# Performance work log

Hardware: AMD Instinct MI355X
Metric: run time of the kernel (lower is better)

Reference implementation:

```python
import jax, jax.numpy as jnp
import numpy as np

IN_FEATURES = 4096
OUT_FEATURES = 4096
BLOCK_SIZE = 64
P = 0.1          # fraction of blocks kept
N_TOKENS = 8192


def setup_inputs() -> dict:
    key = jax.random.key(0)
    k_x, k_w, k_m, k_b = jax.random.split(key, 4)
    x = jax.random.normal(k_x, (N_TOKENS, IN_FEATURES), dtype=jnp.float32)
    # kaiming_uniform_(a=sqrt(5)) on [out, in] -> bound = 1/sqrt(in_features)
    bound = 1.0 / np.sqrt(IN_FEATURES)
    weight = jax.random.uniform(k_w, (OUT_FEATURES, IN_FEATURES), dtype=jnp.float32,
                                minval=-bound, maxval=bound)
    bias = jax.random.uniform(k_b, (OUT_FEATURES,), dtype=jnp.float32,
                              minval=-bound, maxval=bound)
    # Block-structured 0/1 mask: keep each BLOCK_SIZE x BLOCK_SIZE block with prob P
    nb_out, nb_in = OUT_FEATURES // BLOCK_SIZE, IN_FEATURES // BLOCK_SIZE
    block_keep = (jax.random.uniform(k_m, (nb_out, nb_in)) < P).astype(jnp.float32)
    mask = jnp.repeat(jnp.repeat(block_keep, BLOCK_SIZE, axis=0), BLOCK_SIZE, axis=1)
    return {"input": x, "weight": weight, "bias": bias, "mask": mask}


def reference(input, weight, bias, mask):
    # bsr_dense_mm((W*mask).to_sparse_bsr(), x.T).T + bias == x @ (W*mask).T + bias
    masked_w = weight * mask                      # [out, in]
    return input @ masked_w.T + bias              # [N, out]
```

## Files before the change

### kernel.cpp

```cpp
#include <hip/hip_runtime.h>
#include <hip/hip_fp16.h>
#include <cstdint>

#define IN_F   4096
#define OUT_F  4096
#define BS     64
#define NB     64
#define N_TOK  8192
#define TM     256
#define BK     64
#define NMT    (N_TOK / TM)

typedef __attribute__((ext_vector_type(8))) _Float16       f16x8;
typedef __attribute__((ext_vector_type(8))) unsigned short u16x8;
typedef __attribute__((ext_vector_type(4))) float          f32x4;

#define WS_XT_OFF      32768ull
#define WS_XT_BYTES    (2048ull * 32768ull)
#define WS_WT_OFF      (WS_XT_OFF + WS_XT_BYTES)
#define WS_WT_BYTES    (4096ull * 8192ull)
#define WS_NEEDED      (WS_WT_OFF + WS_WT_BYTES)

__global__ void build_meta_kernel(const float* __restrict__ mask,
                                  int* __restrict__ counts,
                                  int* __restrict__ cols) {
    int br = blockIdx.x;
    int bc = threadIdx.x;
    float v = mask[(size_t)(br * BS) * IN_F + (size_t)bc * BS];
    unsigned long long ball = __ballot(v != 0.0f);
    if (v != 0.0f) {
        int pos = __popcll(ball & ((1ull << bc) - 1ull));
        cols[br * NB + pos] = bc;
    }
    if (bc == 0) counts[br] = __popcll(ball);
}

__device__ __forceinline__ u16x8 cvt_f16x8(const float* v) {
    u16x8 o;
#pragma unroll
    for (int j = 0; j < 8; ++j)
        o[j] = __half_as_ushort(__float2half_rn(v[j]));
    return o;
}

__global__ __launch_bounds__(256)
void convert_x_kernel(const float* __restrict__ x, unsigned short* __restrict__ xt) {
    const int t  = blockIdx.x;
    const int mt = t >> 6, kb = t & 63;
    unsigned short* tile = xt + (size_t)t * 16384;
#pragma unroll
    for (int l = 0; l < 8; ++l) {
        int g    = threadIdx.x + l * 256;
        int row  = g >> 3, slot = g & 7;
        const float* src = x + (size_t)(mt * TM + row) * IN_F + kb * BK + slot * 8;
        float4 v0 = *(const float4*)src;
        float4 v1 = *(const float4*)(src + 4);
        float v[8] = {v0.x, v0.y, v0.z, v0.w, v1.x, v1.y, v1.z, v1.w};
        *(u16x8*)&tile[row * 64 + ((slot ^ (row & 7)) << 3)] = cvt_f16x8(v);
    }
}

__global__ __launch_bounds__(256)
void convert_w_kernel(const float* __restrict__ w,
                      const int* __restrict__ counts,
                      const int* __restrict__ cols,
                      unsigned short* __restrict__ wt) {
    const int br = blockIdx.y, si = blockIdx.x;
    if (si >= counts[br]) return;
    const int kb = cols[br * NB + si];
    unsigned short* tile = wt + (size_t)(br * NB + si) * 4096;
#pragma unroll
    for (int l = 0; l < 2; ++l) {
        int g    = threadIdx.x + l * 256;
        int row  = g >> 3, slot = g & 7;
        const float* src = w + (size_t)(br * BS + row) * IN_F + kb * BK + slot * 8;
        float4 v0 = *(const float4*)src;
        float4 v1 = *(const float4*)(src + 4);
        float v[8] = {v0.x, v0.y, v0.z, v0.w, v1.x, v1.y, v1.z, v1.w};
        *(u16x8*)&tile[row * 64 + ((slot ^ (row & 7)) << 3)] = cvt_f16x8(v);
    }
}

__device__ __forceinline__ void gll16(const void* g, void* l) {
    __builtin_amdgcn_global_load_lds(
        (const __attribute__((address_space(1))) unsigned int*)g,
        (__attribute__((address_space(3))) unsigned int*)l, 16, 0, 0);
}

__global__ __launch_bounds__(256, 2)
void bsr_mfma4_kernel(const unsigned short* __restrict__ xt,
                      const unsigned short* __restrict__ wt,
                      const float* __restrict__ bias,
                      const int*   __restrict__ counts,
                      const int*   __restrict__ cols,
                      float* __restrict__ out) {
    __shared__ unsigned short xs[2][TM * BK];
    __shared__ unsigned short wsb[2][BS * BK];

    const int xcd = blockIdx.x & 7;
    const int j   = blockIdx.x >> 3;
    const int mt  = xcd * 4 + (j >> 6);
    const int br  = j & 63;

    const int tid  = threadIdx.x;
    const int lane = tid & 63;
    const int wv   = tid >> 6;
    const int fr   = lane & 15;
    const int kg   = lane >> 4;

    const int  cnt  = counts[br];
    const int* colp = cols + br * NB;

    f32x4 acc[4][4];
#pragma unroll
    for (int a = 0; a < 4; ++a)
#pragma unroll
        for (int b = 0; b < 4; ++b) acc[a][b] = (f32x4)0.0f;

    const char* xbase = (const char*)xt;
    const char* wbase = (const char*)wt;

    auto stage = [&](int si, int bb) {
        const int kb = colp[si];
        const char* xg = xbase + ((size_t)(mt * 64 + kb) << 15);
        const char* wg = wbase + ((size_t)(br * 64 + si) << 13);
        const int bx = wv * 8192;
#pragma unroll
        for (int q = 0; q < 8; ++q)
            gll16(xg + bx + q * 1024 + lane * 16, (char*)xs[bb] + bx + q * 1024);
        const int bw = wv * 2048;
#pragma unroll
        for (int q = 0; q < 2; ++q)
            gll16(wg + bw + q * 1024 + lane * 16, (char*)wsb[bb] + bw + q * 1024);
    };

    int cur = 0;
    if (cnt > 0) stage(0, 0);
    __syncthreads();

    for (int si = 0; si < cnt; ++si) {
        if (si + 1 < cnt) stage(si + 1, cur ^ 1);

#pragma unroll
        for (int ks = 0; ks < 2; ++ks) {
            f16x8 a[4], b[4];
#pragma unroll
            for (int mr = 0; mr < 4; ++mr) {
                int row = wv * 64 + mr * 16 + fr;
                a[mr] = *(const f16x8*)&xs[cur][row * 64 + (((ks * 4 + kg) ^ (row & 7)) << 3)];
            }
#pragma unroll
            for (int nr = 0; nr < 4; ++nr) {
                int row = nr * 16 + fr;
                b[nr] = *(const f16x8*)&wsb[cur][row * 64 + (((ks * 4 + kg) ^ (row & 7)) << 3)];
            }
#pragma unroll
            for (int mr = 0; mr < 4; ++mr)
#pragma unroll
                for (int nr = 0; nr < 4; ++nr)
                    acc[mr][nr] = __builtin_amdgcn_mfma_f32_16x16x32_f16(
                        a[mr], b[nr], acc[mr][nr], 0, 0, 0);
        }
        __syncthreads();
        cur ^= 1;
    }

    const int mbase = mt * TM;
    const int obase = br * BS;
#pragma unroll
    for (int nr = 0; nr < 4; ++nr) {
        float bv = bias[obase + nr * 16 + fr];
#pragma unroll
        for (int mr = 0; mr < 4; ++mr) {
#pragma unroll
            for (int r = 0; r < 4; ++r) {
                int m = mbase + wv * 64 + mr * 16 + kg * 4 + r;
                out[(size_t)m * OUT_F + obase + nr * 16 + fr] = acc[mr][nr][r] + bv;
            }
        }
    }
}

__global__ __launch_bounds__(256, 3)
void bsr_fused_kernel(const float* __restrict__ x,
                      const float* __restrict__ w,
                      const float* __restrict__ bias,
                      const int*   __restrict__ counts,
                      const int*   __restrict__ cols,
                      float* __restrict__ out) {
    __shared__ unsigned short xs[128 * BK];
    __shared__ unsigned short wsb[BS * BK];

    const int mt   = blockIdx.x;
    const int br   = blockIdx.y;
    const int tid  = threadIdx.x;
    const int lane = tid & 63;
    const int wv   = tid >> 6;
    const int fr   = lane & 15;
    const int kg   = lane >> 4;

    const int mbase = mt * 128;
    const int obase = br * BS;
    const int  cnt  = counts[br];
    const int* colp = cols + br * NB;

    f32x4 acc[2][4];
#pragma unroll
    for (int a = 0; a < 2; ++a)
#pragma unroll
        for (int b = 0; b < 4; ++b) acc[a][b] = (f32x4)0.0f;

    for (int si = 0; si < cnt; ++si) {
        const int kbase = colp[si] * BS;
#pragma unroll
        for (int l = 0; l < 4; ++l) {
            int g = tid + l * 256;
            int row = g >> 3, slot = g & 7;
            const float* src = x + (size_t)(mbase + row) * IN_F + kbase + slot * 8;
            float4 v0 = *(const float4*)src;
            float4 v1 = *(const float4*)(src + 4);
            float v[8] = {v0.x, v0.y, v0.z, v0.w, v1.x, v1.y, v1.z, v1.w};
            *(u16x8*)&xs[row * BK + ((slot ^ (row & 7)) << 3)] = cvt_f16x8(v);
        }
#pragma unroll
        for (int l = 0; l < 2; ++l) {
            int g = tid + l * 256;
            int row = g >> 3, slot = g & 7;
            const float* src = w + (size_t)(obase + row) * IN_F + kbase + slot * 8;
            float4 v0 = *(const float4*)src;
            float4 v1 = *(const float4*)(src + 4);
            float v[8] = {v0.x, v0.y, v0.z, v0.w, v1.x, v1.y, v1.z, v1.w};
            *(u16x8*)&wsb[row * BK + ((slot ^ (row & 7)) << 3)] = cvt_f16x8(v);
        }
        __syncthreads();
#pragma unroll
        for (int ks = 0; ks < 2; ++ks) {
            f16x8 a[2], b[4];
#pragma unroll
            for (int mr = 0; mr < 2; ++mr) {
                int row = wv * 32 + mr * 16 + fr;
                a[mr] = *(const f16x8*)&xs[row * BK + (((ks * 4 + kg) ^ (row & 7)) << 3)];
            }
#pragma unroll
            for (int nr = 0; nr < 4; ++nr) {
                int row = nr * 16 + fr;
                b[nr] = *(const f16x8*)&wsb[row * BK + (((ks * 4 + kg) ^ (row & 7)) << 3)];
            }
#pragma unroll
            for (int mr = 0; mr < 2; ++mr)
#pragma unroll
                for (int nr = 0; nr < 4; ++nr)
                    acc[mr][nr] = __builtin_amdgcn_mfma_f32_16x16x32_f16(
                        a[mr], b[nr], acc[mr][nr], 0, 0, 0);
        }
        __syncthreads();
    }

#pragma unroll
    for (int nr = 0; nr < 4; ++nr) {
        float bv = bias[obase + nr * 16 + fr];
#pragma unroll
        for (int mr = 0; mr < 2; ++mr) {
#pragma unroll
            for (int r = 0; r < 4; ++r) {
                int m = mbase + wv * 32 + mr * 16 + kg * 4 + r;
                out[(size_t)m * OUT_F + obase + nr * 16 + fr] = acc[mr][nr][r] + bv;
            }
        }
    }
}

extern "C" void kernel_launch(void* const* d_in, const int* in_sizes, int n_in,
                              void* d_out, int out_size, void* d_ws, size_t ws_size,
                              hipStream_t stream) {
    const float* x    = (const float*)d_in[0];
    const float* w    = (const float*)d_in[1];
    const float* bias = (const float*)d_in[2];
    const float* mask = (const float*)d_in[3];
    float* out = (float*)d_out;

    int* counts = (int*)d_ws;
    int* cols   = (int*)((char*)d_ws + 256);

    build_meta_kernel<<<NB, 64, 0, stream>>>(mask, counts, cols);

    if (ws_size >= WS_NEEDED) {
        unsigned short* xt = (unsigned short*)((char*)d_ws + WS_XT_OFF);
        unsigned short* wt = (unsigned short*)((char*)d_ws + WS_WT_OFF);
        convert_x_kernel<<<NMT * NB, 256, 0, stream>>>(x, xt);
        convert_w_kernel<<<dim3(NB, NB), 256, 0, stream>>>(w, counts, cols, wt);
        bsr_mfma4_kernel<<<NMT * NB, 256, 0, stream>>>(xt, wt, bias, counts, cols, out);
    } else {
        dim3 grid(N_TOK / 128, NB);
        bsr_fused_kernel<<<grid, 256, 0, stream>>>(x, w, bias, counts, cols, out);
    }
}
```

Baseline: 113.9 us.

## Fuse metadata and conversion kernels, recompute mask ballot in-kernel, reorder GEMM blocks

The separate mask-metadata kernel is removed. Each block now derives the kept column bitmask from the mask with a wave ballot and walks it with ffs. The x and w fp16 conversion kernels are merged into a single launch, and the GEMM block-to-tile mapping is changed so each XCD processes paired m-tiles per output block-row, aiming at better L2 locality. This saves launches and a metadata round-trip, at the cost of every block re-reading 64 mask values.

Measured after the change: 118.1 us. +3.7%, slower.

```diff
diff --git a/kernel.cpp b/kernel.cpp
--- a/kernel.cpp
+++ b/kernel.cpp
@@ -15,26 +15,12 @@
 typedef __attribute__((ext_vector_type(8))) unsigned short u16x8;
 typedef __attribute__((ext_vector_type(4))) float          f32x4;
 
-#define WS_XT_OFF      32768ull
+#define WS_XT_OFF      0ull
 #define WS_XT_BYTES    (2048ull * 32768ull)
 #define WS_WT_OFF      (WS_XT_OFF + WS_XT_BYTES)
 #define WS_WT_BYTES    (4096ull * 8192ull)
 #define WS_NEEDED      (WS_WT_OFF + WS_WT_BYTES)
 
-__global__ void build_meta_kernel(const float* __restrict__ mask,
-                                  int* __restrict__ counts,
-                                  int* __restrict__ cols) {
-    int br = blockIdx.x;
-    int bc = threadIdx.x;
-    float v = mask[(size_t)(br * BS) * IN_F + (size_t)bc * BS];
-    unsigned long long ball = __ballot(v != 0.0f);
-    if (v != 0.0f) {
-        int pos = __popcll(ball & ((1ull << bc) - 1ull));
-        cols[br * NB + pos] = bc;
-    }
-    if (bc == 0) counts[br] = __popcll(ball);
-}
-
 __device__ __forceinline__ u16x8 cvt_f16x8(const float* v) {
     u16x8 o;
 #pragma unroll
@@ -43,41 +29,56 @@
     return o;
 }
 
+__device__ __forceinline__ unsigned long long mask_ballot(
+        const float* __restrict__ mask, int br, int lane) {
+    float mv = mask[(size_t)(br * BS) * IN_F + (size_t)lane * BS];
+    return __ballot(mv != 0.0f);
+}
+
 __global__ __launch_bounds__(256)
-void convert_x_kernel(const float* __restrict__ x, unsigned short* __restrict__ xt) {
-    const int t  = blockIdx.x;
-    const int mt = t >> 6, kb = t & 63;
-    unsigned short* tile = xt + (size_t)t * 16384;
-#pragma unroll
-    for (int l = 0; l < 8; ++l) {
-        int g    = threadIdx.x + l * 256;
-        int row  = g >> 3, slot = g & 7;
-        const float* src = x + (size_t)(mt * TM + row) * IN_F + kb * BK + slot * 8;
-        float4 v0 = *(const float4*)src;
-        float4 v1 = *(const float4*)(src + 4);
-        float v[8] = {v0.x, v0.y, v0.z, v0.w, v1.x, v1.y, v1.z, v1.w};
-        *(u16x8*)&tile[row * 64 + ((slot ^ (row & 7)) << 3)] = cvt_f16x8(v);
-    }
-}
-
-__global__ __launch_bounds__(256)
-void convert_w_kernel(const float* __restrict__ w,
-                      const int* __restrict__ counts,
-                      const int* __restrict__ cols,
-                      unsigned short* __restrict__ wt) {
-    const int br = blockIdx.y, si = blockIdx.x;
-    if (si >= counts[br]) return;
-    const int kb = cols[br * NB + si];
-    unsigned short* tile = wt + (size_t)(br * NB + si) * 4096;
-#pragma unroll
-    for (int l = 0; l < 2; ++l) {
-        int g    = threadIdx.x + l * 256;
-        int row  = g >> 3, slot = g & 7;
-        const float* src = w + (size_t)(br * BS + row) * IN_F + kb * BK + slot * 8;
-        float4 v0 = *(const float4*)src;
-        float4 v1 = *(const float4*)(src + 4);
-        float v[8] = {v0.x, v0.y, v0.z, v0.w, v1.x, v1.y, v1.z, v1.w};
-        *(u16x8*)&tile[row * 64 + ((slot ^ (row & 7)) << 3)] = cvt_f16x8(v);
+void convert_all_kernel(const float* __restrict__ x,
+                        const float* __restrict__ w,
+                        const float* __restrict__ mask,
+                        unsigned short* __restrict__ xt,
+                        unsigned short* __restrict__ wt) {
+    const int b = blockIdx.x;
+    if (b < 2048) {
+        const int xcd = b & 7;
+        const int j   = b >> 3;
+        const int mt  = xcd * 4 + (j >> 6);
+        const int kb  = j & 63;
+        unsigned short* tile = xt + (size_t)(mt * 64 + kb) * 16384;
+#pragma unroll
+        for (int l = 0; l < 8; ++l) {
+            int g    = threadIdx.x + l * 256;
+            int row  = g >> 3, slot = g & 7;
+            const float* src = x + (size_t)(mt * TM + row) * IN_F + kb * BK + slot * 8;
+            float4 v0 = *(const float4*)src;
+            float4 v1 = *(const float4*)(src + 4);
+            float v[8] = {v0.x, v0.y, v0.z, v0.w, v1.x, v1.y, v1.z, v1.w};
+            *(u16x8*)&tile[row * 64 + ((slot ^ (row & 7)) << 3)] = cvt_f16x8(v);
+        }
+    } else {
+        const int wb   = b - 2048;
+        const int br   = wb >> 6, si = wb & 63;
+        const int lane = threadIdx.x & 63;
+        unsigned long long ball = mask_ballot(mask, br, lane);
+        if (si >= __popcll(ball)) return;
+        bool fl = ((ball >> lane) & 1ull) &&
+                  (__popcll(ball & ((1ull << lane) - 1ull)) == si);
+        unsigned long long m2 = __ballot(fl);
+        const int kb = __ffsll(m2) - 1;
+        unsigned short* tile = wt + (size_t)(br * NB + si) * 4096;
+#pragma unroll
+        for (int l = 0; l < 2; ++l) {
+            int g    = threadIdx.x + l * 256;
+            int row  = g >> 3, slot = g & 7;
+            const float* src = w + (size_t)(br * BS + row) * IN_F + kb * BK + slot * 8;
+            float4 v0 = *(const float4*)src;
+            float4 v1 = *(const float4*)(src + 4);
+            float v[8] = {v0.x, v0.y, v0.z, v0.w, v1.x, v1.y, v1.z, v1.w};
+            *(u16x8*)&tile[row * 64 + ((slot ^ (row & 7)) << 3)] = cvt_f16x8(v);
+        }
     }
 }
 
@@ -88,19 +89,21 @@
 }
 
 __global__ __launch_bounds__(256, 2)
-void bsr_mfma4_kernel(const unsigned short* __restrict__ xt,
+void bsr_mfma5_kernel(const unsigned short* __restrict__ xt,
                       const unsigned short* __restrict__ wt,
                       const float* __restrict__ bias,
-                      const int*   __restrict__ counts,
-                      const int*   __restrict__ cols,
+                      const float* __restrict__ mask,
                       float* __restrict__ out) {
     __shared__ unsigned short xs[2][TM * BK];
     __shared__ unsigned short wsb[2][BS * BK];
 
-    const int xcd = blockIdx.x & 7;
-    const int j   = blockIdx.x >> 3;
-    const int mt  = xcd * 4 + (j >> 6);
-    const int br  = j & 63;
+    const int b     = blockIdx.x;
+    const int xcd   = b & 7;
+    const int j     = b >> 3;
+    const int phase = j >> 7;
+    const int idx   = j & 127;
+    const int br    = idx >> 1;
+    const int mt    = xcd * 4 + phase * 2 + (idx & 1);
 
     const int tid  = threadIdx.x;
     const int lane = tid & 63;
@@ -108,20 +111,19 @@
     const int fr   = lane & 15;
     const int kg   = lane >> 4;
 
-    const int  cnt  = counts[br];
-    const int* colp = cols + br * NB;
+    unsigned long long ball = mask_ballot(mask, br, lane);
+    const int cnt = __popcll(ball);
 
     f32x4 acc[4][4];
 #pragma unroll
     for (int a = 0; a < 4; ++a)
 #pragma unroll
-        for (int b = 0; b < 4; ++b) acc[a][b] = (f32x4)0.0f;
+        for (int c = 0; c < 4; ++c) acc[a][c] = (f32x4)0.0f;
 
     const char* xbase = (const char*)xt;
     const char* wbase = (const char*)wt;
 
-    auto stage = [&](int si, int bb) {
-        const int kb = colp[si];
+    auto stage = [&](int kb, int si, int bb) {
         const char* xg = xbase + ((size_t)(mt * 64 + kb) << 15);
         const char* wg = wbase + ((size_t)(br * 64 + si) << 13);
         const int bx = wv * 8192;
@@ -134,16 +136,25 @@
             gll16(wg + bw + q * 1024 + lane * 16, (char*)wsb[bb] + bw + q * 1024);
     };
 
+    unsigned long long rem = ball;
     int cur = 0;
-    if (cnt > 0) stage(0, 0);
+    if (cnt > 0) {
+        int kb0 = __ffsll(rem) - 1;
+        rem &= rem - 1;
+        stage(kb0, 0, 0);
+    }
     __syncthreads();
 
     for (int si = 0; si < cnt; ++si) {
-        if (si + 1 < cnt) stage(si + 1, cur ^ 1);
+        if (si + 1 < cnt) {
+            int kbn = __ffsll(rem) - 1;
+            rem &= rem - 1;
+            stage(kbn, si + 1, cur ^ 1);
+        }
 
 #pragma unroll
         for (int ks = 0; ks < 2; ++ks) {
-            f16x8 a[4], b[4];
+            f16x8 a[4], bfr[4];
 #pragma unroll
             for (int mr = 0; mr < 4; ++mr) {
                 int row = wv * 64 + mr * 16 + fr;
@@ -152,14 +163,14 @@
 #pragma unroll
             for (int nr = 0; nr < 4; ++nr) {
                 int row = nr * 16 + fr;
-                b[nr] = *(const f16x8*)&wsb[cur][row * 64 + (((ks * 4 + kg) ^ (row & 7)) << 3)];
+                bfr[nr] = *(const f16x8*)&wsb[cur][row * 64 + (((ks * 4 + kg) ^ (row & 7)) << 3)];
             }
 #pragma unroll
             for (int mr = 0; mr < 4; ++mr)
 #pragma unroll
                 for (int nr = 0; nr < 4; ++nr)
                     acc[mr][nr] = __builtin_amdgcn_mfma_f32_16x16x32_f16(
-                        a[mr], b[nr], acc[mr][nr], 0, 0, 0);
+                        a[mr], bfr[nr], acc[mr][nr], 0, 0, 0);
         }
         __syncthreads();
         cur ^= 1;
@@ -185,8 +196,7 @@
 void bsr_fused_kernel(const float* __restrict__ x,
                       const float* __restrict__ w,
                       const float* __restrict__ bias,
-                      const int*   __restrict__ counts,
-                      const int*   __restrict__ cols,
+                      const float* __restrict__ mask,
                       float* __restrict__ out) {
     __shared__ unsigned short xs[128 * BK];
     __shared__ unsigned short wsb[BS * BK];
@@ -201,17 +211,21 @@
 
     const int mbase = mt * 128;
     const int obase = br * BS;
-    const int  cnt  = counts[br];
-    const int* colp = cols + br * NB;
+
+    unsigned long long ball = mask_ballot(mask, br, lane);
+    const int cnt = __popcll(ball);
+    unsigned long long rem = ball;
 
     f32x4 acc[2][4];
 #pragma unroll
     for (int a = 0; a < 2; ++a)
 #pragma unroll
-        for (int b = 0; b < 4; ++b) acc[a][b] = (f32x4)0.0f;
+        for (int c = 0; c < 4; ++c) acc[a][c] = (f32x4)0.0f;
 
     for (int si = 0; si < cnt; ++si) {
-        const int kbase = colp[si] * BS;
+        const int kb = __ffsll(rem) - 1;
+        rem &= rem - 1;
+        const int kbase = kb * BS;
 #pragma unroll
         for (int l = 0; l < 4; ++l) {
             int g = tid + l * 256;
@@ -235,7 +249,7 @@
         __syncthreads();
 #pragma unroll
         for (int ks = 0; ks < 2; ++ks) {
-            f16x8 a[2], b[4];
+            f16x8 a[2], bfr[4];
 #pragma unroll
             for (int mr = 0; mr < 2; ++mr) {
                 int row = wv * 32 + mr * 16 + fr;
@@ -244,14 +258,14 @@
 #pragma unroll
             for (int nr = 0; nr < 4; ++nr) {
                 int row = nr * 16 + fr;
-                b[nr] = *(const f16x8*)&wsb[row * BK + (((ks * 4 + kg) ^ (row & 7)) << 3)];
+                bfr[nr] = *(const f16x8*)&wsb[row * BK + (((ks * 4 + kg) ^ (row & 7)) << 3)];
             }
 #pragma unroll
             for (int mr = 0; mr < 2; ++mr)
 #pragma unroll
                 for (int nr = 0; nr < 4; ++nr)
                     acc[mr][nr] = __builtin_amdgcn_mfma_f32_16x16x32_f16(
-                        a[mr], b[nr], acc[mr][nr], 0, 0, 0);
+                        a[mr], bfr[nr], acc[mr][nr], 0, 0, 0);
         }
         __syncthreads();
     }
@@ -279,19 +293,13 @@
     const float* mask = (const float*)d_in[3];
     float* out = (float*)d_out;
 
-    int* counts = (int*)d_ws;
-    int* cols   = (int*)((char*)d_ws + 256);
-
-    build_meta_kernel<<<NB, 64, 0, stream>>>(mask, counts, cols);
-
     if (ws_size >= WS_NEEDED) {
         unsigned short* xt = (unsigned short*)((char*)d_ws + WS_XT_OFF);
         unsigned short* wt = (unsigned short*)((char*)d_ws + WS_WT_OFF);
-        convert_x_kernel<<<NMT * NB, 256, 0, stream>>>(x, xt);
-        convert_w_kernel<<<dim3(NB, NB), 256, 0, stream>>>(w, counts, cols, wt);
-        bsr_mfma4_kernel<<<NMT * NB, 256, 0, stream>>>(xt, wt, bias, counts, cols, out);
+        convert_all_kernel<<<2048 + NB * NB, 256, 0, stream>>>(x, w, mask, xt, wt);
+        bsr_mfma5_kernel<<<NMT * NB, 256, 0, stream>>>(xt, wt, bias, mask, out);
     } else {
         dim3 grid(N_TOK / 128, NB);
-        bsr_fused_kernel<<<grid, 256, 0, stream>>>(x, w, bias, counts, cols, out);
-    }
-}
+        bsr_fused_kernel<<<grid, 256, 0, stream>>>(x, w, bias, mask, out);
+    }
+}
```
